# Performance work log

Measured on AMD Instinct MI355X. Metric: run time of the kernel, lower is better.

Reference implementation:

```python
import jax, jax.numpy as jnp
import numpy as np

MIN_CURV = 1e-06
MIN_NORM = 1e-15

def _norm(x):
    return jnp.clip(jnp.linalg.norm(x, axis=-1, keepdims=True), MIN_NORM, None)

def lorentz_expmap0(v, c):
    sqrt_c = jnp.sqrt(c)
    vn = _norm(v)
    x0 = jnp.cosh(sqrt_c * vn) / sqrt_c
    xs = jnp.sinh(sqrt_c * vn) * v / (sqrt_c * vn)
    return jnp.concatenate([x0, xs], axis=-1)

def lorentz_logmap0(x, c):
    sqrt_c = jnp.sqrt(c)
    x0 = x[..., 0:1]
    xs = x[..., 1:]
    xs_norm = _norm(xs)
    theta = jnp.arccosh(jnp.clip(sqrt_c * x0, 1.0 + 1e-07, None))
    return theta / (sqrt_c * xs_norm) * xs

def lorentz_project(x, c):
    spatial = x[..., 1:]
    sq = jnp.sum(spatial * spatial, axis=-1, keepdims=True)
    x0 = jnp.clip(jnp.sqrt(sq + 1.0 / c), MIN_NORM, None)
    return jnp.concatenate([x0, spatial], axis=-1)

def givens_rotation(x, angles):
    x0 = x[..., 0:1]
    xs = x[..., 1:]
    cos_a = jnp.cos(angles)
    sin_a = jnp.sin(angles)
    xe = xs[..., 0::2]
    xo = xs[..., 1::2]
    ne = cos_a * xe - sin_a * xo
    no = sin_a * xe + cos_a * xo
    xr = jnp.stack([ne, no], axis=-1).reshape(xs.shape)
    return jnp.concatenate([x0, xr], axis=-1)

def setup_inputs() -> dict:
    key = jax.random.key(0)
    ks = jax.random.split(key, 16)
    N_NODE, E, B = 50000, 500000, 64
    IN_DIM, OUT_DIM, ATTN_DIM, N_REL = 128, 128, 128, 200
    N_EMB = 2 * N_REL + 1  # 401
    hidden = jax.random.normal(ks[0], (N_NODE, IN_DIM), dtype=jnp.float32)
    q_sub = jax.random.randint(ks[1], (B,), 0, N_NODE)
    q_rel = jax.random.randint(ks[2], (B,), 0, N_EMB)
    r_idx = jax.random.randint(ks[3], (E,), 0, B)
    rel = jax.random.randint(ks[4], (E,), 0, N_EMB)
    sub = jax.random.randint(ks[5], (E,), 0, N_NODE)
    obj = jax.random.randint(ks[6], (E,), 0, N_NODE)
    zeros = jnp.zeros((E,), dtype=jnp.int32)
    edges = jnp.stack([r_idx, zeros, rel, zeros, sub, obj], axis=1)
    rela_embed = jax.random.normal(ks[7], (N_EMB, IN_DIM), dtype=jnp.float32)
    rel_angles = jax.random.uniform(ks[8], (N_EMB, IN_DIM // 2), minval=-0.1, maxval=0.1, dtype=jnp.float32)
    curvature = jnp.array(1.0, dtype=jnp.float32)
    Ws_w = jax.random.normal(ks[9], (ATTN_DIM, IN_DIM), dtype=jnp.float32) * 0.05
    Wr_w = jax.random.normal(ks[10], (ATTN_DIM, IN_DIM), dtype=jnp.float32) * 0.05
    Wqr_w = jax.random.normal(ks[11], (ATTN_DIM, IN_DIM), dtype=jnp.float32) * 0.05
    Wqr_b = jax.random.normal(ks[12], (ATTN_DIM,), dtype=jnp.float32) * 0.05
    Wattn_w = jax.random.normal(ks[13], (1, ATTN_DIM), dtype=jnp.float32) * 0.05
    Wh_w = jax.random.normal(ks[14], (OUT_DIM, IN_DIM), dtype=jnp.float32) * 0.05
    return {"hidden": hidden, "rela_embed": rela_embed, "rel_angles": rel_angles,
            "curvature": curvature, "Ws_w": Ws_w, "Wr_w": Wr_w, "Wqr_w": Wqr_w,
            "Wqr_b": Wqr_b, "Wattn_w": Wattn_w, "Wh_w": Wh_w,
            "q_sub": q_sub, "q_rel": q_rel, "edges": edges,
            "n_node": N_NODE, "old_nodes_new_idx": jnp.arange(N_NODE)}

def reference(hidden, rela_embed, rel_angles, curvature, Ws_w, Wr_w, Wqr_w, Wqr_b,
              Wattn_w, Wh_w, q_sub, q_rel, edges, n_node, old_nodes_new_idx):
    sub = edges[:, 4]
    rel = edges[:, 2]
    obj = edges[:, 5]
    r_idx = edges[:, 0]
    hs = hidden[sub]                      # [E, in_dim]
    hr = rela_embed[rel]                  # [E, in_dim]
    h_qr = rela_embed[q_rel][r_idx]       # [E, in_dim]
    pre = jax.nn.relu(hs @ Ws_w.T + hr @ Wr_w.T + h_qr @ Wqr_w.T + Wqr_b)
    alpha = jax.nn.sigmoid(pre @ Wattn_w.T)  # [E, 1]
    c = jnp.clip(curvature, MIN_CURV, None)
    mess_tangent = hs + hr
    mess_L = lorentz_expmap0(mess_tangent, c)          # [E, in_dim+1]
    mess_L = givens_rotation(mess_L, rel_angles[rel])
    mess2 = lorentz_logmap0(mess_L, c)                 # [E, in_dim]
    message = mess2 * alpha
    message_agg = jax.ops.segment_sum(message, obj, num_segments=n_node)
    a = message_agg @ Wh_w.T                           # [n_node, out_dim]
    a_L = lorentz_expmap0(a, c)
    # act is identity; project back to hyperboloid and log-map
    a_L = lorentz_project(jnp.concatenate([a_L[..., 0:1], a_L[..., 1:]], axis=-1), c)
    hidden_new = lorentz_logmap0(a_L, c)
    return hidden_new
```

## Files before the change

kernel.cpp:

```cpp
#include <hip/hip_runtime.h>
#include <math.h>

#define D 128
#define CAP 36

typedef _Float16 f16x8 __attribute__((ext_vector_type(8)));
typedef _Float16 f16x4 __attribute__((ext_vector_type(4)));
typedef _Float16 f16x2 __attribute__((ext_vector_type(2)));
typedef float    f32x4 __attribute__((ext_vector_type(4)));

union H8 { f16x8 v; f16x4 q[2]; f16x2 p[4]; _Float16 f[8]; };
union H4 { f16x4 v; f16x2 p[2]; _Float16 f[4]; };

__device__ __forceinline__ float fdot2f(f16x2 a, f16x2 b, float c){
  return __builtin_amdgcn_fdot2(a, b, c, false);
}
__device__ __forceinline__ f16x2 relu2(f16x2 x){
  f16x2 r;
  r[0] = x[0] > (_Float16)0 ? x[0] : (_Float16)0;
  r[1] = x[1] > (_Float16)0 ? x[1] : (_Float16)0;
  return r;
}
__device__ __forceinline__ float rsum32(float v){
  v += __shfl_xor(v, 16);
  v += __shfl_xor(v, 8);
  v += __shfl_xor(v, 4);
  v += __shfl_xor(v, 2);
  v += __shfl_xor(v, 1);
  return v;
}


__device__ __forceinline__ void hgemm_core16(const _Float16* __restrict__ A,
                                             const _Float16* __restrict__ W,
                                             int arow, f32x4 acc[8], int quad, int lo){
  #pragma unroll
  for (int kt=0;kt<4;kt++){
    f16x8 a = *(const f16x8*)(A + (size_t)arow*D + kt*32 + quad*8);
    #pragma unroll
    for (int nt=0;nt<8;nt++){
      f16x8 b = *(const f16x8*)(W + (size_t)(nt*16 + lo)*D + kt*32 + quad*8);
      acc[nt] = __builtin_amdgcn_mfma_f32_16x16x32_f16(a, b, acc[nt], 0, 0, 0);
    }
  }
}

__device__ __forceinline__ void store_wpart(_Float16* __restrict__ O, f32x4 acc[8],
                                            int m0, int quad, int lo, int M){
  int r0 = m0 + quad*4;
  #pragma unroll
  for (int i=0;i<4;i++){
    int r = r0 + i;
    if (r < M){
      H4 s1, s2;
      #pragma unroll
      for (int nt=0;nt<4;nt++){
        s1.f[nt] = (_Float16)acc[nt][i];
        s2.f[nt] = (_Float16)acc[nt+4][i];
      }
      *(f16x4*)(O + (size_t)r*256 + lo*16 + 4)  = s1.v;
      *(f16x4*)(O + (size_t)r*256 + lo*16 + 12) = s2.v;
    }
  }
}

__global__ __launch_bounds__(256) void k_prep(
    const float* __restrict__ rela, const float* __restrict__ rel_angles,
    const float* __restrict__ Ws, const float* __restrict__ Wr,
    const float* __restrict__ Wh, const float* __restrict__ Wqr,
    const float* __restrict__ Wqr_b, const int* __restrict__ q_rel,
    _Float16* __restrict__ rela16, _Float16* __restrict__ relhq,
    _Float16* __restrict__ relcs, _Float16* __restrict__ Ws16,
    _Float16* __restrict__ Wr16, _Float16* __restrict__ Wh16,
    _Float16* __restrict__ hqw16, int* __restrict__ cnt,
    int NEMB, int NN, int PA){
  __shared__ float emb[D];
  int b = blockIdx.x;
  int t = threadIdx.x;
  if (b < PA){
    int idx = b*256 + t;
    int T1 = NEMB*32;
    if (idx < T1){
      int r = idx >> 5, l = idx & 31;
      float4 hv = *(const float4*)(rela + (size_t)r*D + l*4);
      f16x4 h = { (_Float16)hv.x, (_Float16)hv.y, (_Float16)hv.z, (_Float16)hv.w };
      *(f16x4*)(rela16 + (size_t)r*D + l*4) = h;
      *(f16x4*)(relhq  + (size_t)r*256 + l*8) = h;
      float2 an = *(const float2*)(rel_angles + (size_t)r*(D/2) + l*2);
      float c0 = cosf(an.x), s0 = sinf(an.x);
      float c1 = cosf(an.y), s1 = sinf(an.y);
      H8 cs;
      cs.f[0]=(_Float16)c0; cs.f[1]=(_Float16)(-s0); cs.f[2]=(_Float16)s0; cs.f[3]=(_Float16)c0;
      cs.f[4]=(_Float16)c1; cs.f[5]=(_Float16)(-s1); cs.f[6]=(_Float16)s1; cs.f[7]=(_Float16)c1;
      *(f16x8*)(relcs + (size_t)r*256 + l*8) = cs.v;
      return;
    }
    int j = idx - T1;
    if (j < 3*D*D/4){
      const float* src = (j < 4096) ? Ws : (j < 8192) ? Wr : Wh;
      _Float16*    dst = (j < 4096) ? Ws16 : (j < 8192) ? Wr16 : Wh16;
      int o = (j & 4095)*4;
      float4 v = *(const float4*)(src + o);
      f16x4 h = { (_Float16)v.x, (_Float16)v.y, (_Float16)v.z, (_Float16)v.w };
      *(f16x4*)(dst + o) = h;
      return;
    }
    j -= 3*D*D/4;
    if (j < NN) cnt[j] = 0;
  } else {
    int bb = b - PA;
    if (t < D) emb[t] = rela[(size_t)q_rel[bb]*D + t];
    __syncthreads();
    if (t < D){
      float acc = Wqr_b[t];
      #pragma unroll 8
      for (int k=0;k<D;k++) acc += emb[k]*Wqr[t*D + k];
      int p = ((t & 15) << 3) + (t >> 4);
      hqw16[bb*D + p] = (_Float16)acc;
    }
  }
}

__global__ __launch_bounds__(256) void k_mega(
    const int* __restrict__ edges, int* __restrict__ cnt, int* __restrict__ bucket,
    int E, const float* __restrict__ hidden, const _Float16* __restrict__ Ws16,
    _Float16* __restrict__ hw16, int NN,
    const _Float16* __restrict__ rela16, const _Float16* __restrict__ Wr16,
    _Float16* __restrict__ relhq, int NEMB, int SB, int GH){
  int b = blockIdx.x;
  if (b < SB){
    int e0 = (b*256 + threadIdx.x)*4;
    if (e0 >= E) return;
    if (e0 + 3 < E){
      const int4* q = (const int4*)(edges + (size_t)e0*6);
      int4 q0=q[0], q1=q[1], q2=q[2], q3=q[3], q4=q[4], q5=q[5];
      int key0 = q1.x | (q0.z << 17) | (q0.x << 26);
      int key1 = q2.z | (q2.x << 17) | (q1.z << 26);
      int key2 = q4.x | (q3.z << 17) | (q3.x << 26);
      int key3 = q5.z | (q5.x << 17) | (q4.z << 26);
      int p0 = atomicAdd(cnt + q1.y, 1);
      int p1 = atomicAdd(cnt + q2.w, 1);
      int p2 = atomicAdd(cnt + q4.y, 1);
      int p3 = atomicAdd(cnt + q5.w, 1);
      if (p0 < CAP) bucket[q1.y*CAP + p0] = key0;
      if (p1 < CAP) bucket[q2.w*CAP + p1] = key1;
      if (p2 < CAP) bucket[q4.y*CAP + p2] = key2;
      if (p3 < CAP) bucket[q5.w*CAP + p3] = key3;
    } else {
      for (int u=0; u<4; u++){
        int e = e0 + u;
        if (e < E){
          const int* er = edges + (size_t)e*6;
          int key = er[4] | (er[2] << 17) | (er[0] << 26);
          int pos = atomicAdd(cnt + er[5], 1);
          if (pos < CAP) bucket[er[5]*CAP + pos] = key;
        }
      }
    }
  } else if (b < SB + GH){
    int bb = b - SB;
    int wave = threadIdx.x >> 6;
    int lane = threadIdx.x & 63;
    int quad = lane >> 4, lo = lane & 15;
    int m0 = bb*64 + wave*16;
    int arow = min(m0 + lo, NN-1);
    f32x4 acc[8];
    #pragma unroll
    for (int nt=0;nt<8;nt++) acc[nt] = (f32x4){0.f,0.f,0.f,0.f};
    H8 hpack[4];
    #pragma unroll
    for (int kt=0;kt<4;kt++){
      float4 a0 = *(const float4*)(hidden + (size_t)arow*D + kt*32 + quad*8);
      float4 a1 = *(const float4*)(hidden + (size_t)arow*D + kt*32 + quad*8 + 4);
      H8 a;
      a.f[0]=(_Float16)a0.x; a.f[1]=(_Float16)a0.y; a.f[2]=(_Float16)a0.z; a.f[3]=(_Float16)a0.w;
      a.f[4]=(_Float16)a1.x; a.f[5]=(_Float16)a1.y; a.f[6]=(_Float16)a1.z; a.f[7]=(_Float16)a1.w;
      hpack[kt] = a;
      #pragma unroll
      for (int nt=0;nt<8;nt++){
        f16x8 bb2 = *(const f16x8*)(Ws16 + (size_t)(nt*16 + lo)*D + kt*32 + quad*8);
        acc[nt] = __builtin_amdgcn_mfma_f32_16x16x32_f16(a.v, bb2, acc[nt], 0, 0, 0);
      }
    }
    if (m0 + lo < NN){
      #pragma unroll
      for (int kt=0;kt<4;kt++){
        int g = kt*8 + quad*2;
        *(f16x4*)(hw16 + (size_t)arow*256 + g*8)     = hpack[kt].q[0];
        *(f16x4*)(hw16 + (size_t)arow*256 + (g+1)*8) = hpack[kt].q[1];
      }
    }
    store_wpart(hw16, acc, m0, quad, lo, NN);
  } else {
    int bb = b - SB - GH;
    int wave = threadIdx.x >> 6;
    int lane = threadIdx.x & 63;
    int quad = lane >> 4, lo = lane & 15;
    int m0 = bb*64 + wave*16;
    int arow = min(m0 + lo, NEMB-1);
    f32x4 acc[8];
    #pragma unroll
    for (int nt=0;nt<8;nt++) acc[nt] = (f32x4){0.f,0.f,0.f,0.f};
    hgemm_core16(rela16, Wr16, arow, acc, quad, lo);
    store_wpart(relhq, acc, m0, quad, lo, NEMB);
  }
}

__device__ __forceinline__ void edge_op(int key,
    const _Float16* __restrict__ hw16, const _Float16* __restrict__ relcs,
    const _Float16* __restrict__ relhq, const _Float16* __restrict__ hqw16,
    unsigned lh8, unsigned lh4, f16x2 wa01, f16x2 wa23,
    float& ax, float& ay, float& az, float& aw){
  unsigned sub = key & 0x1FFFF, rel = ((unsigned)key >> 17) & 0x1FF, ri = (unsigned)key >> 26;
  H8 hw; hw.v = *(const f16x8*)(hw16  + (sub << 8) + lh8);
  H8 cs; cs.v = *(const f16x8*)(relcs + (rel << 8) + lh8);
  H8 hq; hq.v = *(const f16x8*)(relhq + (rel << 8) + lh8);
  H4 qw; qw.v = *(const f16x4*)(hqw16 + (ri  << 7) + lh4);
  f16x2 t01 = relu2(hw.p[2] + hq.p[2] + qw.p[0]);
  f16x2 t23 = relu2(hw.p[3] + hq.p[3] + qw.p[1]);
  float s = fdot2f(t01, wa01, fdot2f(t23, wa23, 0.f));
  s = rsum32(s);
  float al = __builtin_amdgcn_rcpf(1.f + __expf(-s));
  f16x2 v01 = hw.p[0] + hq.p[0];
  f16x2 v23 = hw.p[1] + hq.p[1];
  ax += al * fdot2f(cs.p[0], v01, 0.f);
  ay += al * fdot2f(cs.p[1], v01, 0.f);
  az += al * fdot2f(cs.p[2], v23, 0.f);
  aw += al * fdot2f(cs.p[3], v23, 0.f);
}

__global__ __launch_bounds__(256) void k_aggregate(
    const _Float16* __restrict__ hw16, const _Float16* __restrict__ relcs,
    const _Float16* __restrict__ relhq, const _Float16* __restrict__ hqw16,
    const float* __restrict__ Wattn, const int* __restrict__ cnt,
    const int* __restrict__ bucket, _Float16* __restrict__ agg16, int NN){
  int t = threadIdx.x;
  int half = t >> 5, l = t & 31;
  int n = blockIdx.x*8 + half;
  if (n >= NN) return;
  unsigned lh8 = (unsigned)l*8, lh4 = (unsigned)l*4;
  unsigned p0 = (unsigned)l*4;
  float w0 = Wattn[(((p0+0)&7)<<4) + ((p0+0)>>3)];
  float w1 = Wattn[(((p0+1)&7)<<4) + ((p0+1)>>3)];
  float w2 = Wattn[(((p0+2)&7)<<4) + ((p0+2)>>3)];
  float w3 = Wattn[(((p0+3)&7)<<4) + ((p0+3)>>3)];
  f16x2 wa01 = { (_Float16)w0, (_Float16)w1 };
  f16x2 wa23 = { (_Float16)w2, (_Float16)w3 };

  int deg = min(cnt[n], CAP);
  const int* bk = bucket + n*CAP;
  float ax=0.f, ay=0.f, az=0.f, aw=0.f;

  int i = 0;
  for (; i+4 <= deg; i += 4){
    int4 q = *(const int4*)(bk + i);
    edge_op(q.x, hw16, relcs, relhq, hqw16, lh8, lh4, wa01, wa23, ax, ay, az, aw);
    edge_op(q.y, hw16, relcs, relhq, hqw16, lh8, lh4, wa01, wa23, ax, ay, az, aw);
    edge_op(q.z, hw16, relcs, relhq, hqw16, lh8, lh4, wa01, wa23, ax, ay, az, aw);
    edge_op(q.w, hw16, relcs, relhq, hqw16, lh8, lh4, wa01, wa23, ax, ay, az, aw);
  }
  for (; i < deg; i++)
    edge_op(bk[i], hw16, relcs, relhq, hqw16, lh8, lh4, wa01, wa23, ax, ay, az, aw);

  f16x4 o = { (_Float16)ax, (_Float16)ay, (_Float16)az, (_Float16)aw };
  *(f16x4*)(agg16 + ((size_t)n << 7) + lh4) = o;
}

__global__ __launch_bounds__(256) void k_hgemm0(const _Float16* __restrict__ A,
                                                const _Float16* __restrict__ W,
                                                float* __restrict__ O, int M){
  int wave = threadIdx.x >> 6;
  int lane = threadIdx.x & 63;
  int quad = lane >> 4, lo = lane & 15;
  int m0 = blockIdx.x*64 + wave*16;
  int arow = min(m0 + lo, M-1);
  f32x4 acc[8];
  #pragma unroll
  for (int nt=0;nt<8;nt++) acc[nt] = (f32x4){0.f,0.f,0.f,0.f};
  hgemm_core16(A, W, arow, acc, quad, lo);
  int r0 = m0 + quad*4;
  #pragma unroll
  for (int nt=0;nt<8;nt++){
    int c = nt*16 + lo;
    #pragma unroll
    for (int i=0;i<4;i++){
      int r = r0 + i;
      if (r < M) O[(size_t)r*D + c] = acc[nt][i];
    }
  }
}

extern "C" void kernel_launch(void* const* d_in, const int* in_sizes, int n_in,
                              void* d_out, int out_size, void* d_ws, size_t ws_size,
                              hipStream_t stream){
  const float* hidden     = (const float*)d_in[0];
  const float* rela       = (const float*)d_in[1];
  const float* rel_angles = (const float*)d_in[2];
  const float* Ws         = (const float*)d_in[4];
  const float* Wr         = (const float*)d_in[5];
  const float* Wqr        = (const float*)d_in[6];
  const float* Wqr_b      = (const float*)d_in[7];
  const float* Wattn      = (const float*)d_in[8];
  const float* Wh         = (const float*)d_in[9];
  const int*   q_rel      = (const int*)d_in[11];
  const int*   edges      = (const int*)d_in[12];

  int NN   = in_sizes[0] / D;
  int NEMB = in_sizes[1] / D;
  int B    = in_sizes[11];
  int E    = in_sizes[12] / 6;

  char* p = (char*)d_ws;
  auto alloc = [&](size_t bytes)->char*{
    char* r = p; p += (bytes + 255) & ~(size_t)255; return r;
  };
  _Float16* hw16   = (_Float16*)alloc((size_t)NN*256*2);
  _Float16* agg16  = (_Float16*)alloc((size_t)NN*D*2);
  _Float16* rela16 = (_Float16*)alloc((size_t)NEMB*D*2);
  _Float16* relhq  = (_Float16*)alloc((size_t)NEMB*256*2);
  _Float16* relcs  = (_Float16*)alloc((size_t)NEMB*256*2);
  _Float16* hqw16  = (_Float16*)alloc((size_t)B*D*2);
  _Float16* Ws16   = (_Float16*)alloc((size_t)D*D*2);
  _Float16* Wr16   = (_Float16*)alloc((size_t)D*D*2);
  _Float16* Wh16   = (_Float16*)alloc((size_t)D*D*2);
  int*      cnt    = (int*)alloc((size_t)NN*4);
  int*      bucket = (int*)alloc((size_t)NN*CAP*4);

  int smallN = NEMB*32 + 3*D*D/4 + NN;
  int PA = (smallN + 255)/256;
  k_prep<<<PA + B, 256, 0, stream>>>(rela, rel_angles, Ws, Wr, Wh, Wqr, Wqr_b,
                                     q_rel, rela16, relhq, relcs, Ws16, Wr16,
                                     Wh16, hqw16, cnt, NEMB, NN, PA);

  int SB = (E + 1023)/1024;
  int GH = (NN + 63)/64;
  int G1 = (NEMB + 63)/64;
  k_mega<<<SB + GH + G1, 256, 0, stream>>>(edges, cnt, bucket, E, hidden, Ws16,
                                           hw16, NN, rela16, Wr16, relhq, NEMB,
                                           SB, GH);

  k_aggregate<<<(NN+7)/8, 256, 0, stream>>>(hw16, relcs, relhq, hqw16,
                                            Wattn, cnt, bucket, agg16, NN);
  k_hgemm0<<<(NN+63)/64, 256, 0, stream>>>(agg16, Wh16, (float*)d_out, NN);
}
```

Baseline: 239.1 us.

## Fuse edge aggregation with the Wh output GEMM via shared-memory tile

The aggregation kernel and the final Wh GEMM are merged into one kernel. Each block now aggregates 16 nodes (two passes of 8 half-waves), stages the fp16 aggregates in an LDS tile, then runs MFMA 16x16x32 with each wave computing two column tiles. This removes the agg16 round trip through global memory and one kernel launch. The cost is a block-wide barrier, twice the serial aggregation work per thread, and Wh being re-read by every block.

```diff
diff --git a/kernel.cpp b/kernel.cpp
--- a/kernel.cpp
+++ b/kernel.cpp
@@ -229,15 +229,17 @@
   aw += al * fdot2f(cs.p[3], v23, 0.f);
 }
 
-__global__ __launch_bounds__(256) void k_aggregate(
+#define ASTR 136
+
+__global__ __launch_bounds__(256) void k_aggfin(
     const _Float16* __restrict__ hw16, const _Float16* __restrict__ relcs,
     const _Float16* __restrict__ relhq, const _Float16* __restrict__ hqw16,
     const float* __restrict__ Wattn, const int* __restrict__ cnt,
-    const int* __restrict__ bucket, _Float16* __restrict__ agg16, int NN){
+    const int* __restrict__ bucket, const _Float16* __restrict__ Wh16,
+    float* __restrict__ out, int NN){
+  __shared__ _Float16 As[16*ASTR];
   int t = threadIdx.x;
   int half = t >> 5, l = t & 31;
-  int n = blockIdx.x*8 + half;
-  if (n >= NN) return;
   unsigned lh8 = (unsigned)l*8, lh4 = (unsigned)l*4;
   unsigned p0 = (unsigned)l*4;
   float w0 = Wattn[(((p0+0)&7)<<4) + ((p0+0)>>3)];
@@ -247,45 +249,56 @@
   f16x2 wa01 = { (_Float16)w0, (_Float16)w1 };
   f16x2 wa23 = { (_Float16)w2, (_Float16)w3 };
 
-  int deg = min(cnt[n], CAP);
-  const int* bk = bucket + n*CAP;
-  float ax=0.f, ay=0.f, az=0.f, aw=0.f;
-
-  int i = 0;
-  for (; i+4 <= deg; i += 4){
-    int4 q = *(const int4*)(bk + i);
-    edge_op(q.x, hw16, relcs, relhq, hqw16, lh8, lh4, wa01, wa23, ax, ay, az, aw);
-    edge_op(q.y, hw16, relcs, relhq, hqw16, lh8, lh4, wa01, wa23, ax, ay, az, aw);
-    edge_op(q.z, hw16, relcs, relhq, hqw16, lh8, lh4, wa01, wa23, ax, ay, az, aw);
-    edge_op(q.w, hw16, relcs, relhq, hqw16, lh8, lh4, wa01, wa23, ax, ay, az, aw);
-  }
-  for (; i < deg; i++)
-    edge_op(bk[i], hw16, relcs, relhq, hqw16, lh8, lh4, wa01, wa23, ax, ay, az, aw);
-
-  f16x4 o = { (_Float16)ax, (_Float16)ay, (_Float16)az, (_Float16)aw };
-  *(f16x4*)(agg16 + ((size_t)n << 7) + lh4) = o;
-}
-
-__global__ __launch_bounds__(256) void k_hgemm0(const _Float16* __restrict__ A,
-                                                const _Float16* __restrict__ W,
-                                                float* __restrict__ O, int M){
-  int wave = threadIdx.x >> 6;
-  int lane = threadIdx.x & 63;
+  int nbase = blockIdx.x * 16;
+
+  #pragma unroll
+  for (int srep = 0; srep < 2; srep++){
+    int s = half + srep*8;
+    int n = nbase + s;
+    float ax=0.f, ay=0.f, az=0.f, aw=0.f;
+    if (n < NN){
+      int deg = min(cnt[n], CAP);
+      const int* bk = bucket + n*CAP;
+      int i = 0;
+      for (; i+4 <= deg; i += 4){
+        int4 q = *(const int4*)(bk + i);
+        edge_op(q.x, hw16, relcs, relhq, hqw16, lh8, lh4, wa01, wa23, ax, ay, az, aw);
+        edge_op(q.y, hw16, relcs, relhq, hqw16, lh8, lh4, wa01, wa23, ax, ay, az, aw);
+        edge_op(q.z, hw16, relcs, relhq, hqw16, lh8, lh4, wa01, wa23, ax, ay, az, aw);
+        edge_op(q.w, hw16, relcs, relhq, hqw16, lh8, lh4, wa01, wa23, ax, ay, az, aw);
+      }
+      for (; i < deg; i++)
+        edge_op(bk[i], hw16, relcs, relhq, hqw16, lh8, lh4, wa01, wa23, ax, ay, az, aw);
+    }
+    H4 o;
+    o.f[0] = (_Float16)ax; o.f[1] = (_Float16)ay;
+    o.f[2] = (_Float16)az; o.f[3] = (_Float16)aw;
+    *(f16x4*)(As + s*ASTR + lh4) = o.v;
+  }
+  __syncthreads();
+
+  int wv = t >> 6, lane = t & 63;
   int quad = lane >> 4, lo = lane & 15;
-  int m0 = blockIdx.x*64 + wave*16;
-  int arow = min(m0 + lo, M-1);
-  f32x4 acc[8];
-  #pragma unroll
-  for (int nt=0;nt<8;nt++) acc[nt] = (f32x4){0.f,0.f,0.f,0.f};
-  hgemm_core16(A, W, arow, acc, quad, lo);
-  int r0 = m0 + quad*4;
-  #pragma unroll
-  for (int nt=0;nt<8;nt++){
-    int c = nt*16 + lo;
+  f32x4 acc[2];
+  acc[0] = (f32x4){0.f,0.f,0.f,0.f};
+  acc[1] = (f32x4){0.f,0.f,0.f,0.f};
+  #pragma unroll
+  for (int kt=0;kt<4;kt++){
+    f16x8 a = *(const f16x8*)(As + lo*ASTR + kt*32 + quad*8);
+    #pragma unroll
+    for (int u=0;u<2;u++){
+      int nt = wv*2 + u;
+      f16x8 b = *(const f16x8*)(Wh16 + (size_t)(nt*16 + lo)*D + kt*32 + quad*8);
+      acc[u] = __builtin_amdgcn_mfma_f32_16x16x32_f16(a, b, acc[u], 0, 0, 0);
+    }
+  }
+  #pragma unroll
+  for (int u=0;u<2;u++){
+    int c = (wv*2 + u)*16 + lo;
     #pragma unroll
     for (int i=0;i<4;i++){
-      int r = r0 + i;
-      if (r < M) O[(size_t)r*D + c] = acc[nt][i];
+      int r = nbase + quad*4 + i;
+      if (r < NN) out[(size_t)r*D + c] = acc[u][i];
     }
   }
 }
@@ -315,7 +328,6 @@
     char* r = p; p += (bytes + 255) & ~(size_t)255; return r;
   };
   _Float16* hw16   = (_Float16*)alloc((size_t)NN*256*2);
-  _Float16* agg16  = (_Float16*)alloc((size_t)NN*D*2);
   _Float16* rela16 = (_Float16*)alloc((size_t)NEMB*D*2);
   _Float16* relhq  = (_Float16*)alloc((size_t)NEMB*256*2);
   _Float16* relcs  = (_Float16*)alloc((size_t)NEMB*256*2);
@@ -339,7 +351,6 @@
                                            hw16, NN, rela16, Wr16, relhq, NEMB,
                                            SB, GH);
 
-  k_aggregate<<<(NN+7)/8, 256, 0, stream>>>(hw16, relcs, relhq, hqw16,
-                                            Wattn, cnt, bucket, agg16, NN);
-  k_hgemm0<<<(NN+63)/64, 256, 0, stream>>>(agg16, Wh16, (float*)d_out, NN);
-}
+  k_aggfin<<<(NN+15)/16, 256, 0, stream>>>(hw16, relcs, relhq, hqw16, Wattn,
+                                           cnt, bucket, Wh16, (float*)d_out, NN);
+}
```

Result: no change. 243.5 us (+1.8%).
